# Performance work log

Measured on AMD Instinct MI355X. Metric: run time of the kernel, lower is better.

Reference implementation:

```python
import jax, jax.numpy as jnp
import numpy as np

VOCAB, H, HEADS, S, FF = 100, 8, 2, 6, 16
HD = H // HEADS  # head_dim = 4
EPS = 1e-5


def _layernorm(x, g, b):
    mu = jnp.mean(x, axis=-1, keepdims=True)
    var = jnp.mean((x - mu) ** 2, axis=-1, keepdims=True)
    return (x - mu) * jax.lax.rsqrt(var + EPS) * g + b


def setup_inputs() -> dict:
    key = jax.random.key(0)
    ks = jax.random.split(key, 20)
    B = 262144
    d = {
        'input_ids': jax.random.randint(ks[0], (B, S), 0, VOCAB),
        'tok_emb': jax.random.normal(ks[1], (VOCAB, H), jnp.float32) * 0.02,
        'pos_emb': jax.random.normal(ks[2], (S, H), jnp.float32) * 0.02,
        'Wq': jax.random.normal(ks[3], (H, H), jnp.float32) * 0.1,
        'bq': jnp.zeros((H,), jnp.float32),
        'Wk': jax.random.normal(ks[4], (H, H), jnp.float32) * 0.1,
        'bk': jnp.zeros((H,), jnp.float32),
        'Wv': jax.random.normal(ks[5], (H, H), jnp.float32) * 0.1,
        'bv': jnp.zeros((H,), jnp.float32),
        'Wo': jax.random.normal(ks[6], (H, H), jnp.float32) * 0.1,
        'bo': jnp.zeros((H,), jnp.float32),
        'W1': jax.random.normal(ks[7], (FF, H), jnp.float32) * 0.1,
        'b1': jnp.zeros((FF,), jnp.float32),
        'W2': jax.random.normal(ks[8], (H, FF), jnp.float32) * 0.1,
        'b2': jnp.zeros((H,), jnp.float32),
        'g1': jnp.ones((H,), jnp.float32),
        'be1': jnp.zeros((H,), jnp.float32),
        'g2': jnp.ones((H,), jnp.float32),
        'be2': jnp.zeros((H,), jnp.float32),
    }
    return d


def reference(input_ids, tok_emb, pos_emb, Wq, bq, Wk, bk, Wv, bv, Wo, bo,
              W1, b1, W2, b2, g1, be1, g2, be2):
    B, Sq = input_ids.shape
    x = tok_emb[input_ids] + pos_emb[None, :, :]  # [B,S,H]
    q = x @ Wq.T + bq
    k = x @ Wk.T + bk
    v = x @ Wv.T + bv
    # split heads: [B, heads, S, head_dim]
    q = q.reshape(B, Sq, HEADS, HD).transpose(0, 2, 1, 3)
    k = k.reshape(B, Sq, HEADS, HD).transpose(0, 2, 1, 3)
    v = v.reshape(B, Sq, HEADS, HD).transpose(0, 2, 1, 3)
    scores = jnp.einsum('bhsd,bhtd->bhst', q, k) / (HD ** 0.5)
    probs = jax.nn.softmax(scores, axis=-1)
    attn = jnp.einsum('bhst,bhtd->bhsd', probs, v)
    attn = attn.transpose(0, 2, 1, 3).reshape(B, Sq, H)
    attn = attn @ Wo.T + bo
    h = _layernorm(x + attn, g1, be1)
    ffn = jax.nn.gelu(h @ W1.T + b1, approximate=False) @ W2.T + b2
    return _layernorm(h + ffn, g2, be2)
```

## Files before the change

### kernel.cpp

```cpp
#include <hip/hip_runtime.h>

#define TT_S 6
#define TT_H 8
#define TT_FF 16
#define WAVES_PER_BLK 4
#define BLK (WAVES_PER_BLK * 64)
#define SEQ_PER_WAVE 10
#define SEQ_PER_BLK (WAVES_PER_BLK * SEQ_PER_WAVE)
#define SEQ_STRIDE_U 52
#define WAVE_STRIDE_U (SEQ_PER_WAVE * SEQ_STRIDE_U + 8)

#define WQH  0
#define WKH  32
#define WVH  64
#define WOH  96
#define W1H  128
#define W2H  192
#define POSH 256
#define TOKH 288

typedef __fp16   h2_t  __attribute__((ext_vector_type(2)));
typedef __fp16   h8_t  __attribute__((ext_vector_type(8)));
typedef _Float16 f16x2 __attribute__((ext_vector_type(2)));

__device__ __forceinline__ unsigned pk2(float a, float b) {
  h2_t h = __builtin_amdgcn_cvt_pkrtz(a, b);
  return __builtin_bit_cast(unsigned, h);
}
__device__ __forceinline__ h2_t pk2h(float a, float b) {
  return __builtin_amdgcn_cvt_pkrtz(a, b);
}
__device__ __forceinline__ h2_t bch(unsigned u) {
  return __builtin_bit_cast(h2_t, u);
}

#if __has_builtin(__builtin_amdgcn_fdot2)
__device__ __forceinline__ float dot2f(h2_t a, h2_t b, float c) {
  return __builtin_amdgcn_fdot2(__builtin_bit_cast(f16x2, a),
                                __builtin_bit_cast(f16x2, b), c, false);
}
#else
__device__ __forceinline__ float dot2f(h2_t a, h2_t b, float c) {
  return fmaf((float)a[0], (float)b[0], fmaf((float)a[1], (float)b[1], c));
}
#endif

__global__ void tt_prep(const float* __restrict__ Wq, const float* __restrict__ Wk,
                        const float* __restrict__ Wv, const float* __restrict__ Wo,
                        const float* __restrict__ W1, const float* __restrict__ W2,
                        const float* __restrict__ pos, const float* __restrict__ tok,
                        unsigned* __restrict__ ws)
{
  const int i = threadIdx.x;
  if (i < 128) {
    const float* Wm = (i < 32) ? Wq : (i < 64) ? Wk : (i < 96) ? Wv : Wo;
    const int p = i & 31;
    ws[i] = pk2(Wm[2*p], Wm[2*p+1]);
  }
  if (i < 64) {
    ws[W1H + i] = pk2(W1[2*i], W1[2*i+1]);
    ws[W2H + i] = pk2(W2[2*i], W2[2*i+1]);
  }
  if (i < 24) ws[POSH + i] = pk2(pos[2*i], pos[2*i+1]);
  if (i < 400) ws[TOKH + i] = pk2(tok[2*i], tok[2*i+1]);
}

__global__ __launch_bounds__(BLK, 8) void tt_fused(
    const int* __restrict__ ids,
    const unsigned* __restrict__ wsu,
    const float* __restrict__ bq, const float* __restrict__ bk,
    const float* __restrict__ bv, const float* __restrict__ bo,
    const float* __restrict__ b1, const float* __restrict__ b2,
    const float* __restrict__ g1, const float* __restrict__ be1,
    const float* __restrict__ g2, const float* __restrict__ be2,
    float* __restrict__ out, int B)
{
  __shared__ __align__(16) unsigned s_kv[WAVES_PER_BLK * WAVE_STRIDE_U];

  const int tid = threadIdx.x;
  const int wv  = tid >> 6;
  const int ln  = tid & 63;
  const int slr = ln / 6;
  const int t   = ln - slr * 6;
  const int seq_g = blockIdx.x * SEQ_PER_BLK + wv * SEQ_PER_WAVE + slr;
  if (ln >= 60 || seq_g >= B) return;

  const size_t gidx = (size_t)seq_g * TT_S + t;
  const int id = ids[gidx];

  uint4 tw = ((const uint4*)(wsu + TOKH))[id];
  uint4 pw = ((const uint4*)(wsu + POSH))[t];
  h2_t xs0 = bch(tw.x) + bch(pw.x);
  h2_t xs1 = bch(tw.y) + bch(pw.y);
  h2_t xs2 = bch(tw.z) + bch(pw.z);
  h2_t xs3 = bch(tw.w) + bch(pw.w);

  float xf[TT_H];
  xf[0] = (float)xs0[0]; xf[1] = (float)xs0[1];
  xf[2] = (float)xs1[0]; xf[3] = (float)xs1[1];
  xf[4] = (float)xs2[0]; xf[5] = (float)xs2[1];
  xf[6] = (float)xs3[0]; xf[7] = (float)xs3[1];

  unsigned* kvbase = s_kv + wv * WAVE_STRIDE_U + slr * SEQ_STRIDE_U;

  {
    float kr[TT_H], vr[TT_H];
    #pragma unroll
    for (int i = 0; i < TT_H; ++i) {
      float ak = bk[i], av = bv[i];
      ak = dot2f(xs0, bch(wsu[WKH + i*4 + 0]), ak);
      ak = dot2f(xs1, bch(wsu[WKH + i*4 + 1]), ak);
      ak = dot2f(xs2, bch(wsu[WKH + i*4 + 2]), ak);
      ak = dot2f(xs3, bch(wsu[WKH + i*4 + 3]), ak);
      av = dot2f(xs0, bch(wsu[WVH + i*4 + 0]), av);
      av = dot2f(xs1, bch(wsu[WVH + i*4 + 1]), av);
      av = dot2f(xs2, bch(wsu[WVH + i*4 + 2]), av);
      av = dot2f(xs3, bch(wsu[WVH + i*4 + 3]), av);
      kr[i] = ak; vr[i] = av;
    }
    unsigned* kvp = kvbase + t * 8;
    uint4 w0, w1;
    w0.x = pk2(kr[0], kr[1]); w0.y = pk2(kr[2], kr[3]);
    w0.z = pk2(kr[4], kr[5]); w0.w = pk2(kr[6], kr[7]);
    w1.x = pk2(vr[0], vr[1]); w1.y = pk2(vr[2], vr[3]);
    w1.z = pk2(vr[4], vr[5]); w1.w = pk2(vr[6], vr[7]);
    ((uint4*)kvp)[0] = w0;
    ((uint4*)kvp)[1] = w1;
  }
  __builtin_amdgcn_wave_barrier();

  h2_t qh[4];
  #pragma unroll
  for (int i = 0; i < 4; ++i) {
    float a0 = bq[2*i], a1 = bq[2*i+1];
    a0 = dot2f(xs0, bch(wsu[WQH + (2*i)*4 + 0]), a0);
    a0 = dot2f(xs1, bch(wsu[WQH + (2*i)*4 + 1]), a0);
    a0 = dot2f(xs2, bch(wsu[WQH + (2*i)*4 + 2]), a0);
    a0 = dot2f(xs3, bch(wsu[WQH + (2*i)*4 + 3]), a0);
    a1 = dot2f(xs0, bch(wsu[WQH + (2*i+1)*4 + 0]), a1);
    a1 = dot2f(xs1, bch(wsu[WQH + (2*i+1)*4 + 1]), a1);
    a1 = dot2f(xs2, bch(wsu[WQH + (2*i+1)*4 + 2]), a1);
    a1 = dot2f(xs3, bch(wsu[WQH + (2*i+1)*4 + 3]), a1);
    qh[i] = pk2h(a0 * 0.7213475204f, a1 * 0.7213475204f);
  }

  float acc[TT_H] = {0.f,0.f,0.f,0.f,0.f,0.f,0.f,0.f};
  float sum0 = 0.f, sum1 = 0.f;
  const uint4* kvb = (const uint4*)kvbase;
  #pragma unroll
  for (int t2 = 0; t2 < TT_S; ++t2) {
    uint4 kw = kvb[t2*2];
    uint4 vw = kvb[t2*2+1];
    float d0 = dot2f(qh[0], bch(kw.x), 0.f);
    d0 = dot2f(qh[1], bch(kw.y), d0);
    float d1 = dot2f(qh[2], bch(kw.z), 0.f);
    d1 = dot2f(qh[3], bch(kw.w), d1);
    float e0 = __builtin_amdgcn_exp2f(d0);
    float e1 = __builtin_amdgcn_exp2f(d1);
    sum0 += e0; sum1 += e1;
    h8_t vh = __builtin_bit_cast(h8_t, vw);
    acc[0] = fmaf(e0, (float)vh[0], acc[0]);
    acc[1] = fmaf(e0, (float)vh[1], acc[1]);
    acc[2] = fmaf(e0, (float)vh[2], acc[2]);
    acc[3] = fmaf(e0, (float)vh[3], acc[3]);
    acc[4] = fmaf(e1, (float)vh[4], acc[4]);
    acc[5] = fmaf(e1, (float)vh[5], acc[5]);
    acc[6] = fmaf(e1, (float)vh[6], acc[6]);
    acc[7] = fmaf(e1, (float)vh[7], acc[7]);
  }
  h2_t ah[4];
  {
    float inv0 = __builtin_amdgcn_rcpf(sum0);
    float inv1 = __builtin_amdgcn_rcpf(sum1);
    ah[0] = pk2h(acc[0]*inv0, acc[1]*inv0);
    ah[1] = pk2h(acc[2]*inv0, acc[3]*inv0);
    ah[2] = pk2h(acc[4]*inv1, acc[5]*inv1);
    ah[3] = pk2h(acc[6]*inv1, acc[7]*inv1);
  }

  float r[TT_H];
  float mu = 0.f;
  #pragma unroll
  for (int i = 0; i < TT_H; ++i) {
    float o = bo[i];
    o = dot2f(ah[0], bch(wsu[WOH + i*4 + 0]), o);
    o = dot2f(ah[1], bch(wsu[WOH + i*4 + 1]), o);
    o = dot2f(ah[2], bch(wsu[WOH + i*4 + 2]), o);
    o = dot2f(ah[3], bch(wsu[WOH + i*4 + 3]), o);
    r[i] = xf[i] + o;
    mu += r[i];
  }
  mu *= 0.125f;
  float var = 0.f;
  #pragma unroll
  for (int i = 0; i < TT_H; ++i) { float d = r[i] - mu; var = fmaf(d, d, var); }
  float rin = __builtin_amdgcn_rsqf(fmaf(var, 0.125f, 1e-5f));
  float mc = mu * rin;
  float hr[TT_H];
  #pragma unroll
  for (int i = 0; i < TT_H; ++i)
    hr[i] = fmaf(fmaf(r[i], rin, -mc), g1[i], be1[i]);
  h2_t hh[4];
  hh[0] = pk2h(hr[0], hr[1]);
  hh[1] = pk2h(hr[2], hr[3]);
  hh[2] = pk2h(hr[4], hr[5]);
  hh[3] = pk2h(hr[6], hr[7]);

  h2_t fh[8];
  #pragma unroll
  for (int f = 0; f < TT_FF; f += 2) {
    float u0 = b1[f], u1 = b1[f+1];
    u0 = dot2f(hh[0], bch(wsu[W1H + f*4 + 0]), u0);
    u0 = dot2f(hh[1], bch(wsu[W1H + f*4 + 1]), u0);
    u0 = dot2f(hh[2], bch(wsu[W1H + f*4 + 2]), u0);
    u0 = dot2f(hh[3], bch(wsu[W1H + f*4 + 3]), u0);
    u1 = dot2f(hh[0], bch(wsu[W1H + f*4 + 4]), u1);
    u1 = dot2f(hh[1], bch(wsu[W1H + f*4 + 5]), u1);
    u1 = dot2f(hh[2], bch(wsu[W1H + f*4 + 6]), u1);
    u1 = dot2f(hh[3], bch(wsu[W1H + f*4 + 7]), u1);
    float e0 = __builtin_amdgcn_exp2f(u0 * fmaf(0.1029432f, u0*u0, 2.3022072f));
    float e1 = __builtin_amdgcn_exp2f(u1 * fmaf(0.1029432f, u1*u1, 2.3022072f));
    float g0 = fmaf(-u0, __builtin_amdgcn_rcpf(e0 + 1.0f), u0);
    float g1v = fmaf(-u1, __builtin_amdgcn_rcpf(e1 + 1.0f), u1);
    fh[f>>1] = pk2h(g0, g1v);
  }

  float r2[TT_H];
  float mu2 = 0.f;
  #pragma unroll
  for (int i = 0; i < TT_H; ++i) {
    float y = b2[i];
    y = dot2f(fh[0], bch(wsu[W2H + i*8 + 0]), y);
    y = dot2f(fh[1], bch(wsu[W2H + i*8 + 1]), y);
    y = dot2f(fh[2], bch(wsu[W2H + i*8 + 2]), y);
    y = dot2f(fh[3], bch(wsu[W2H + i*8 + 3]), y);
    y = dot2f(fh[4], bch(wsu[W2H + i*8 + 4]), y);
    y = dot2f(fh[5], bch(wsu[W2H + i*8 + 5]), y);
    y = dot2f(fh[6], bch(wsu[W2H + i*8 + 6]), y);
    y = dot2f(fh[7], bch(wsu[W2H + i*8 + 7]), y);
    r2[i] = hr[i] + y;
    mu2 += r2[i];
  }
  mu2 *= 0.125f;
  float var2 = 0.f;
  #pragma unroll
  for (int i = 0; i < TT_H; ++i) { float d = r2[i] - mu2; var2 = fmaf(d, d, var2); }
  float rin2 = __builtin_amdgcn_rsqf(fmaf(var2, 0.125f, 1e-5f));
  float mc2 = mu2 * rin2;

  float res[TT_H];
  #pragma unroll
  for (int i = 0; i < TT_H; ++i)
    res[i] = fmaf(fmaf(r2[i], rin2, -mc2), g2[i], be2[i]);
  float* op = out + gidx * TT_H;
  float4 v0; v0.x = res[0]; v0.y = res[1]; v0.z = res[2]; v0.w = res[3];
  float4 v1; v1.x = res[4]; v1.y = res[5]; v1.z = res[6]; v1.w = res[7];
  ((float4*)op)[0] = v0;
  ((float4*)op)[1] = v1;
}

extern "C" void kernel_launch(void* const* d_in, const int* in_sizes, int n_in,
                              void* d_out, int out_size, void* d_ws, size_t ws_size,
                              hipStream_t stream) {
  const int*   ids = (const int*)  d_in[0];
  const float* tok = (const float*)d_in[1];
  const float* pos = (const float*)d_in[2];
  const float* Wq  = (const float*)d_in[3];
  const float* bq  = (const float*)d_in[4];
  const float* Wk  = (const float*)d_in[5];
  const float* bk  = (const float*)d_in[6];
  const float* Wv  = (const float*)d_in[7];
  const float* bv  = (const float*)d_in[8];
  const float* Wo  = (const float*)d_in[9];
  const float* bo  = (const float*)d_in[10];
  const float* W1  = (const float*)d_in[11];
  const float* b1  = (const float*)d_in[12];
  const float* W2  = (const float*)d_in[13];
  const float* b2  = (const float*)d_in[14];
  const float* g1  = (const float*)d_in[15];
  const float* be1 = (const float*)d_in[16];
  const float* g2  = (const float*)d_in[17];
  const float* be2 = (const float*)d_in[18];
  float* out = (float*)d_out;
  unsigned* ws = (unsigned*)d_ws;

  hipLaunchKernelGGL(tt_prep, dim3(1), dim3(512), 0, stream,
                     Wq, Wk, Wv, Wo, W1, W2, pos, tok, ws);

  const int B = in_sizes[0] / TT_S;
  const int grid = (B + SEQ_PER_BLK - 1) / SEQ_PER_BLK;
  hipLaunchKernelGGL(tt_fused, dim3(grid), dim3(BLK), 0, stream,
                     ids, ws, bq, bk, bv, bo, b1, b2,
                     g1, be1, g2, be2, out, B);
}
```

Before: 139.5 us.

## Use packed fp16 attention accumulation, shared reciprocals, and smaller blocks

The attention value accumulation moves from eight fp32 FMAs with per-element fp16-to-fp32 conversions to four packed fp16 multiply-adds. The two softmax reciprocals are merged into one reciprocal of the product, and the GELU's two reciprocals per pair are merged the same way. Blocks also shrink from four to two waves. This trims transcendental and conversion instructions, but fp16 accumulation and the product of sums can lose precision or overflow when the exponentials are large.

```diff
diff --git a/kernel.cpp b/kernel.cpp
--- a/kernel.cpp
+++ b/kernel.cpp
@@ -3,7 +3,7 @@
 #define TT_S 6
 #define TT_H 8
 #define TT_FF 16
-#define WAVES_PER_BLK 4
+#define WAVES_PER_BLK 2
 #define BLK (WAVES_PER_BLK * 64)
 #define SEQ_PER_WAVE 10
 #define SEQ_PER_BLK (WAVES_PER_BLK * SEQ_PER_WAVE)
@@ -20,7 +20,6 @@
 #define TOKH 288
 
 typedef __fp16   h2_t  __attribute__((ext_vector_type(2)));
-typedef __fp16   h8_t  __attribute__((ext_vector_type(8)));
 typedef _Float16 f16x2 __attribute__((ext_vector_type(2)));
 
 __device__ __forceinline__ unsigned pk2(float a, float b) {
@@ -144,7 +143,9 @@
     qh[i] = pk2h(a0 * 0.7213475204f, a1 * 0.7213475204f);
   }
 
-  float acc[TT_H] = {0.f,0.f,0.f,0.f,0.f,0.f,0.f,0.f};
+  h2_t acch[4];
+  acch[0] = h2_t{0.f, 0.f}; acch[1] = h2_t{0.f, 0.f};
+  acch[2] = h2_t{0.f, 0.f}; acch[3] = h2_t{0.f, 0.f};
   float sum0 = 0.f, sum1 = 0.f;
   const uint4* kvb = (const uint4*)kvbase;
   #pragma unroll
@@ -158,24 +159,24 @@
     float e0 = __builtin_amdgcn_exp2f(d0);
     float e1 = __builtin_amdgcn_exp2f(d1);
     sum0 += e0; sum1 += e1;
-    h8_t vh = __builtin_bit_cast(h8_t, vw);
-    acc[0] = fmaf(e0, (float)vh[0], acc[0]);
-    acc[1] = fmaf(e0, (float)vh[1], acc[1]);
-    acc[2] = fmaf(e0, (float)vh[2], acc[2]);
-    acc[3] = fmaf(e0, (float)vh[3], acc[3]);
-    acc[4] = fmaf(e1, (float)vh[4], acc[4]);
-    acc[5] = fmaf(e1, (float)vh[5], acc[5]);
-    acc[6] = fmaf(e1, (float)vh[6], acc[6]);
-    acc[7] = fmaf(e1, (float)vh[7], acc[7]);
+    h2_t e0p = pk2h(e0, e0);
+    h2_t e1p = pk2h(e1, e1);
+    acch[0] = e0p * bch(vw.x) + acch[0];
+    acch[1] = e0p * bch(vw.y) + acch[1];
+    acch[2] = e1p * bch(vw.z) + acch[2];
+    acch[3] = e1p * bch(vw.w) + acch[3];
   }
   h2_t ah[4];
   {
-    float inv0 = __builtin_amdgcn_rcpf(sum0);
-    float inv1 = __builtin_amdgcn_rcpf(sum1);
-    ah[0] = pk2h(acc[0]*inv0, acc[1]*inv0);
-    ah[1] = pk2h(acc[2]*inv0, acc[3]*inv0);
-    ah[2] = pk2h(acc[4]*inv1, acc[5]*inv1);
-    ah[3] = pk2h(acc[6]*inv1, acc[7]*inv1);
+    float rs = __builtin_amdgcn_rcpf(sum0 * sum1);
+    float inv0 = sum1 * rs;
+    float inv1 = sum0 * rs;
+    h2_t i0p = pk2h(inv0, inv0);
+    h2_t i1p = pk2h(inv1, inv1);
+    ah[0] = acch[0] * i0p;
+    ah[1] = acch[1] * i0p;
+    ah[2] = acch[2] * i1p;
+    ah[3] = acch[3] * i1p;
   }
 
   float r[TT_H];
@@ -220,8 +221,11 @@
     u1 = dot2f(hh[3], bch(wsu[W1H + f*4 + 7]), u1);
     float e0 = __builtin_amdgcn_exp2f(u0 * fmaf(0.1029432f, u0*u0, 2.3022072f));
     float e1 = __builtin_amdgcn_exp2f(u1 * fmaf(0.1029432f, u1*u1, 2.3022072f));
-    float g0 = fmaf(-u0, __builtin_amdgcn_rcpf(e0 + 1.0f), u0);
-    float g1v = fmaf(-u1, __builtin_amdgcn_rcpf(e1 + 1.0f), u1);
+    float a0 = e0 + 1.0f;
+    float a1 = e1 + 1.0f;
+    float rp = __builtin_amdgcn_rcpf(a0 * a1);
+    float g0 = fmaf(-u0, a1 * rp, u0);
+    float g1v = fmaf(-u1, a0 * rp, u1);
     fh[f>>1] = pk2h(g0, g1v);
   }
 
```

New measurement: 137.1 us. No clear change (-1.7%).
